# Optimization experiments

Hardware: AMD Instinct MI355X
Metric: run time of the kernel (lower is better)

Reference implementation:

```python
import jax, jax.numpy as jnp
import numpy as np

EPS = 1e-6
OMEGA = 0.1


def setup_inputs() -> dict:
    key = jax.random.key(0)
    k1, k2 = jax.random.split(key)
    n, d, kk = 4096, 128, 4
    inputs = jax.random.uniform(k1, (n, d), dtype=jnp.float32)  # positive so log(sim) is finite
    labels = jax.random.randint(k2, (n, kk), 0, 64, dtype=jnp.int64)
    return {"inputs": inputs, "labels": labels}


def reference(inputs, labels):
    n, kk = labels.shape
    sim = inputs @ inputs.T                      # [n, n]
    logsim = jnp.log(sim + EPS)                  # a_{jk} = log(sim[j,k]+eps)
    targets = labels[:, 0]
    eye = jnp.eye(n, dtype=bool)
    # pos_mask[j,k] = (targets[j] == targets[k]) xor diagonal
    pos = (targets[:, None] == targets[None, :]) & ~eye
    # eq[j,l,i] = (labels[l,i] == targets[j])
    eq = targets[:, None, None] == labels[None, :, :]
    m_idx = jnp.arange(kk)
    cols = kk - 1 - m_idx                        # neg_mask[m] uses label column kk-1-m
    # neg_mask[m][j,l] == 1  <=>  ~eq[j,l,kk-1-m]  AND  (m==0 or eq[j,l,kk-m])
    neq_col = ~eq[:, :, cols]                    # [j,l,m]
    prev_ok = jnp.concatenate(
        [jnp.ones((n, n, 1), dtype=bool), eq[:, :, cols[:-1]]], axis=-1)
    neg = neq_col & prev_ok                      # [j,l,m]
    # loss_pair[m] = log(Omega+eps) - log(Omega^(kk-m+1)+eps)
    lp = jnp.log(OMEGA + EPS) - jnp.log(OMEGA ** (kk - m_idx + 1) + EPS)  # [kk]
    dt = logsim.dtype
    posf = pos.astype(dt)
    negf = neg.astype(dt)
    # term = (a_jk - b_jlm)^2 with b_jlm = logsim[j,l] + 0.1*lp[m]
    # expand: sum_jklm pos*neg*(a^2 - 2ab + b^2), separable over k and (l,m)
    c = posf.sum(1)                              # [j] count of positives
    S1 = (posf * logsim).sum(1)                  # [j] sum a
    S2 = (posf * logsim ** 2).sum(1)             # [j] sum a^2
    b = logsim[:, :, None] + 0.1 * lp[None, None, :]   # [j,l,m]
    Ncnt = negf.sum(1)                           # [j,m]
    T1 = (negf * b).sum(1)                       # [j,m]
    T2 = (negf * b ** 2).sum(1)                  # [j,m]
    loss = (S2[:, None] * Ncnt - 2.0 * S1[:, None] * T1 + c[:, None] * T2).sum()
    return loss
```

## Files before the change

### kernel.cpp

```cpp
#include <hip/hip_runtime.h>
#include <math.h>

constexpr int N  = 4096;
constexpr int D  = 128;
constexpr int TI = 128;
constexpr int TJ = 128;
constexpr int LDK = D + 8;
constexpr int REDSTRIDE = 97;

typedef __attribute__((ext_vector_type(8))) short short8;
typedef __attribute__((ext_vector_type(4))) float floatx4;

__device__ inline unsigned short f2bf(float f) {
  unsigned u = __builtin_bit_cast(unsigned, f);
  u = (u + 0x7FFFu + ((u >> 16) & 1u)) >> 16;
  return (unsigned short)u;
}

__global__ __launch_bounds__(256, 2) void logratio_phaseA(
    const float* __restrict__ inputs, const int* __restrict__ labels,
    float* __restrict__ ws,
    float B0, float B1, float B2, float B3,
    float Q0, float Q1, float Q2, float Q3) {

  __shared__ char smem[2 * 128 * LDK * 2];
  unsigned short* As = (unsigned short*)smem;
  unsigned short* Bs = As + 128 * LDK;

  const int tid = threadIdx.x;
  const int iBase = blockIdx.y * TI;
  const int jBase = blockIdx.x * TJ;

#pragma unroll
  for (int p = 0; p < 16; ++p) {
    const int idx = p * 256 + tid;
    const int row = idx >> 5;
    const int cf  = idx & 31;
    const float4 va = *(const float4*)&inputs[(iBase + row) * D + cf * 4];
    uint2 wa;
    wa.x = (unsigned)f2bf(va.x) | ((unsigned)f2bf(va.y) << 16);
    wa.y = (unsigned)f2bf(va.z) | ((unsigned)f2bf(va.w) << 16);
    *(uint2*)&As[row * LDK + cf * 4] = wa;
    const float4 vb = *(const float4*)&inputs[(jBase + row) * D + cf * 4];
    uint2 wb;
    wb.x = (unsigned)f2bf(vb.x) | ((unsigned)f2bf(vb.y) << 16);
    wb.y = (unsigned)f2bf(vb.z) | ((unsigned)f2bf(vb.w) << 16);
    *(uint2*)&Bs[row * LDK + cf * 4] = wb;
  }
  __syncthreads();

  const int w    = tid >> 6;
  const int lane = tid & 63;
  const int lc   = lane & 15;
  const int quad = lane >> 4;

  floatx4 acc[2][8] = {};

  const unsigned short* Abase = As + (w * 32 + lc) * LDK + quad * 8;
  const unsigned short* Bbase = Bs + lc * LDK + quad * 8;

#pragma unroll
  for (int kb = 0; kb < 4; ++kb) {
    short8 af[2], bfr[8];
    af[0] = *(const short8*)(Abase + kb * 32);
    af[1] = *(const short8*)(Abase + 16 * LDK + kb * 32);
#pragma unroll
    for (int tn = 0; tn < 8; ++tn)
      bfr[tn] = *(const short8*)(Bbase + tn * 16 * LDK + kb * 32);
#pragma unroll
    for (int tm = 0; tm < 2; ++tm)
#pragma unroll
      for (int tn = 0; tn < 8; ++tn)
        acc[tm][tn] = __builtin_amdgcn_mfma_f32_16x16x32_bf16(af[tm], bfr[tn], acc[tm][tn], 0, 0, 0);
  }

  int4 labs[8];
#pragma unroll
  for (int tn = 0; tn < 8; ++tn)
    labs[tn] = ((const int4*)labels)[jBase + tn * 16 + lc];

  __syncthreads();
  float* Red = (float*)smem;

#pragma unroll
  for (int tm = 0; tm < 2; ++tm) {
#pragma unroll
    for (int reg = 0; reg < 4; ++reg) {
      const int row = w * 32 + tm * 16 + quad * 4 + reg;
      const int gi = iBase + row;
      const int ti = labels[gi * 4];

      float a_c = 0.f, a_s1 = 0.f, a_s2 = 0.f;
      float a_A = 0.f, a_B = 0.f, a_C = 0.f;

#pragma unroll
      for (int tn = 0; tn < 8; ++tn) {
        const int gj = jBase + tn * 16 + lc;
        const float sim = acc[tm][tn][reg];
        const float ls  = __logf(sim + 1e-6f);
        const float ls2 = ls * ls;
        const int4 L = labs[tn];
        const bool e0 = (ti == L.x);
        const bool e1 = (ti == L.y);
        const bool e2 = (ti == L.z);
        const bool e3 = (ti == L.w);
        const bool n1 = e3 && !e2;
        const bool n2 = e2 && !e1;
        const bool n3 = e1 && !e0;
        const float g0 = (float)((e3 ? 0 : 1) + (n1 ? 1 : 0) + (n2 ? 1 : 0) + (n3 ? 1 : 0));
        const float gB = (e3 ? (n1 ? B1 : 0.f) : B0) + (n2 ? B2 : 0.f) + (n3 ? B3 : 0.f);
        const float gQ = (e3 ? (n1 ? Q1 : 0.f) : Q0) + (n2 ? Q2 : 0.f) + (n3 ? Q3 : 0.f);
        const float fp = (e0 && (gi != gj)) ? 1.f : 0.f;

        a_c += fp;
        a_s1 = fmaf(fp, ls, a_s1);
        a_s2 = fmaf(fp, ls2, a_s2);
        a_A += g0;
        a_B += fmaf(g0, ls, gB);
        a_C += fmaf(fmaf(g0, ls, 2.f * gB), ls, gQ);
      }

      float* dst = Red + row * REDSTRIDE + lc * 6;
      dst[0] = a_c;  dst[1] = a_s1; dst[2] = a_s2;
      dst[3] = a_A;  dst[4] = a_B;  dst[5] = a_C;
    }
  }
  __syncthreads();

  if (tid < 128) {
    const int row = tid;
    const int gi = iBase + row;
    const float* src = Red + row * REDSTRIDE;
    float s0 = 0.f, s1 = 0.f, s2 = 0.f, s3 = 0.f, s4 = 0.f, s5 = 0.f;
#pragma unroll
    for (int l = 0; l < 16; ++l) {
      s0 += src[l * 6 + 0]; s1 += src[l * 6 + 1]; s2 += src[l * 6 + 2];
      s3 += src[l * 6 + 3]; s4 += src[l * 6 + 4]; s5 += src[l * 6 + 5];
    }
    atomicAdd(&ws[0 * N + gi], s0);
    atomicAdd(&ws[1 * N + gi], s1);
    atomicAdd(&ws[2 * N + gi], s2);
    atomicAdd(&ws[3 * N + gi], s3);
    atomicAdd(&ws[4 * N + gi], s4);
    atomicAdd(&ws[5 * N + gi], s5);
  }
}

__global__ __launch_bounds__(256) void logratio_phaseB(
    const float* __restrict__ ws, float* __restrict__ out) {
  const int i = blockIdx.x * 256 + threadIdx.x;
  const float c  = ws[0 * N + i];
  const float S1 = ws[1 * N + i];
  const float S2 = ws[2 * N + i];
  const float A  = ws[3 * N + i];
  const float B  = ws[4 * N + i];
  const float C  = ws[5 * N + i];
  float v = S2 * A - 2.f * S1 * B + c * C;
#pragma unroll
  for (int m = 32; m >= 1; m >>= 1) v += __shfl_xor(v, m, 64);
  __shared__ float wsum[4];
  if ((threadIdx.x & 63) == 0) wsum[threadIdx.x >> 6] = v;
  __syncthreads();
  if (threadIdx.x == 0)
    atomicAdd(out, wsum[0] + wsum[1] + wsum[2] + wsum[3]);
}

extern "C" void kernel_launch(void* const* d_in, const int* in_sizes, int n_in,
                              void* d_out, int out_size, void* d_ws, size_t ws_size,
                              hipStream_t stream) {
  const float* inputs = (const float*)d_in[0];
  const int* labels = (const int*)d_in[1];
  float* out = (float*)d_out;
  float* ws = (float*)d_ws;

  hipMemsetAsync(d_ws, 0, 6 * N * sizeof(float), stream);
  hipMemsetAsync(d_out, 0, sizeof(float), stream);

  float Bq[4], Qq[4];
  for (int m = 0; m < 4; ++m) {
    const float lpv = logf(0.1f + 1e-6f) - logf(powf(0.1f, (float)(5 - m)) + 1e-6f);
    Bq[m] = 0.1f * lpv;
    Qq[m] = Bq[m] * Bq[m];
  }

  dim3 grid(N / TJ, N / TI);
  logratio_phaseA<<<grid, 256, 0, stream>>>(inputs, labels, ws,
                                            Bq[0], Bq[1], Bq[2], Bq[3],
                                            Qq[0], Qq[1], Qq[2], Qq[3]);
  logratio_phaseB<<<N / 256, 256, 0, stream>>>(ws, out);
}
```

Measured before the change: 91.01 us.

## Compact sparse label matches into per-wave queues and use dense baseline sums

The per-element epilogue now computes only the log-similarity and its square densely. Elements whose label matches are pushed into per-wave LDS queues and processed sparsely as corrections to a baseline assumption of all-negative. Global atomics are replaced by per-block partial slots in the workspace, which removes the workspace memset, and phase B reduces those slots. The queued log values are stored as fp16, and entries beyond a fixed queue capacity are dropped, which can introduce error if matches are dense.

```diff
diff --git a/kernel.cpp b/kernel.cpp
--- a/kernel.cpp
+++ b/kernel.cpp
@@ -1,12 +1,11 @@
 #include <hip/hip_runtime.h>
+#include <hip/hip_fp16.h>
 #include <math.h>
 
-constexpr int N  = 4096;
-constexpr int D  = 128;
-constexpr int TI = 128;
-constexpr int TJ = 128;
+constexpr int N   = 4096;
+constexpr int D   = 128;
 constexpr int LDK = D + 8;
-constexpr int REDSTRIDE = 97;
+constexpr int QCAPW = 1024;
 
 typedef __attribute__((ext_vector_type(8))) short short8;
 typedef __attribute__((ext_vector_type(4))) float floatx4;
@@ -23,13 +22,16 @@
     float B0, float B1, float B2, float B3,
     float Q0, float Q1, float Q2, float Q3) {
 
-  __shared__ char smem[2 * 128 * LDK * 2];
+  __shared__ __align__(16) char smem[2 * 128 * LDK * 2];
   unsigned short* As = (unsigned short*)smem;
   unsigned short* Bs = As + 128 * LDK;
+  float (*rowacc)[8] = (float (*)[8])smem;
+  unsigned* queues   = (unsigned*)(smem + 4096);
+  unsigned* qcnt     = (unsigned*)(smem + 4096 + 16384);
 
   const int tid = threadIdx.x;
-  const int iBase = blockIdx.y * TI;
-  const int jBase = blockIdx.x * TJ;
+  const int iBase = blockIdx.y * 128;
+  const int jBase = blockIdx.x * 128;
 
 #pragma unroll
   for (int p = 0; p < 16; ++p) {
@@ -55,7 +57,6 @@
   const int quad = lane >> 4;
 
   floatx4 acc[2][8] = {};
-
   const unsigned short* Abase = As + (w * 32 + lc) * LDK + quad * 8;
   const unsigned short* Bbase = Bs + lc * LDK + quad * 8;
 
@@ -80,7 +81,12 @@
     labs[tn] = ((const int4*)labels)[jBase + tn * 16 + lc];
 
   __syncthreads();
-  float* Red = (float*)smem;
+
+  for (int z = tid; z < 128 * 8; z += 256) ((float*)rowacc)[z] = 0.f;
+  __syncthreads();
+
+  unsigned wq = 0;
+  unsigned* wqueue = queues + w * QCAPW;
 
 #pragma unroll
   for (int tm = 0; tm < 2; ++tm) {
@@ -89,80 +95,102 @@
       const int row = w * 32 + tm * 16 + quad * 4 + reg;
       const int gi = iBase + row;
       const int ti = labels[gi * 4];
-
-      float a_c = 0.f, a_s1 = 0.f, a_s2 = 0.f;
-      float a_A = 0.f, a_B = 0.f, a_C = 0.f;
-
+      float t0 = 0.f, t1 = 0.f;
 #pragma unroll
       for (int tn = 0; tn < 8; ++tn) {
-        const int gj = jBase + tn * 16 + lc;
-        const float sim = acc[tm][tn][reg];
-        const float ls  = __logf(sim + 1e-6f);
-        const float ls2 = ls * ls;
+        const int col = tn * 16 + lc;
+        const float ls = __logf(acc[tm][tn][reg] + 1e-6f);
+        t0 += ls;
+        t1 = fmaf(ls, ls, t1);
         const int4 L = labs[tn];
-        const bool e0 = (ti == L.x);
-        const bool e1 = (ti == L.y);
-        const bool e2 = (ti == L.z);
-        const bool e3 = (ti == L.w);
-        const bool n1 = e3 && !e2;
-        const bool n2 = e2 && !e1;
-        const bool n3 = e1 && !e0;
-        const float g0 = (float)((e3 ? 0 : 1) + (n1 ? 1 : 0) + (n2 ? 1 : 0) + (n3 ? 1 : 0));
-        const float gB = (e3 ? (n1 ? B1 : 0.f) : B0) + (n2 ? B2 : 0.f) + (n3 ? B3 : 0.f);
-        const float gQ = (e3 ? (n1 ? Q1 : 0.f) : Q0) + (n2 ? Q2 : 0.f) + (n3 ? Q3 : 0.f);
-        const float fp = (e0 && (gi != gj)) ? 1.f : 0.f;
-
-        a_c += fp;
-        a_s1 = fmaf(fp, ls, a_s1);
-        a_s2 = fmaf(fp, ls2, a_s2);
-        a_A += g0;
-        a_B += fmaf(g0, ls, gB);
-        a_C += fmaf(fmaf(g0, ls, 2.f * gB), ls, gQ);
+        const bool match = (ti == L.x) | (ti == L.y) | (ti == L.z) | (ti == L.w);
+        const unsigned long long mk = __ballot(match);
+        if (mk) {
+          const unsigned pfx = __builtin_amdgcn_mbcnt_hi(
+              (unsigned)(mk >> 32), __builtin_amdgcn_mbcnt_lo((unsigned)mk, 0u));
+          if (match) {
+            const unsigned pos = wq + pfx;
+            if (pos < (unsigned)QCAPW)
+              wqueue[pos] = ((unsigned)(row * 128 + col) << 16) |
+                            (unsigned)__half_as_ushort(__float2half(ls));
+          }
+          wq += (unsigned)__popcll(mk);
+        }
       }
-
-      float* dst = Red + row * REDSTRIDE + lc * 6;
-      dst[0] = a_c;  dst[1] = a_s1; dst[2] = a_s2;
-      dst[3] = a_A;  dst[4] = a_B;  dst[5] = a_C;
+#pragma unroll
+      for (int m = 1; m <= 8; m <<= 1) {
+        t0 += __shfl_xor(t0, m, 64);
+        t1 += __shfl_xor(t1, m, 64);
+      }
+      if (lc == 0) { rowacc[row][6] = t0; rowacc[row][7] = t1; }
     }
   }
+  if (lane == 0) qcnt[w] = (wq < (unsigned)QCAPW) ? wq : (unsigned)QCAPW;
+  __syncthreads();
+
+#pragma unroll 1
+  for (int qw = 0; qw < 4; ++qw) {
+    const unsigned qn = qcnt[qw];
+    const unsigned* qq = queues + qw * QCAPW;
+    for (unsigned q = tid; q < qn; q += 256) {
+      const unsigned e = qq[q];
+      const int idx = (int)(e >> 16);
+      const int row = idx >> 7;
+      const int col = idx & 127;
+      const float ls = __half2float(__ushort_as_half((unsigned short)(e & 0xFFFFu)));
+      const int gi = iBase + row, gj = jBase + col;
+      const int ti = labels[gi * 4];
+      const int4 L = ((const int4*)labels)[gj];
+      const bool e0 = (ti == L.x), e1 = (ti == L.y), e2 = (ti == L.z), e3 = (ti == L.w);
+      const float g0 = (e3 ? 0.f : 1.f) + ((e3 && !e2) ? 1.f : 0.f) +
+                       ((e2 && !e1) ? 1.f : 0.f) + ((e1 && !e0) ? 1.f : 0.f);
+      const float gB = (e3 ? (!e2 ? B1 : 0.f) : B0) + ((e2 && !e1) ? B2 : 0.f) + ((e1 && !e0) ? B3 : 0.f);
+      const float gQ = (e3 ? (!e2 ? Q1 : 0.f) : Q0) + ((e2 && !e1) ? Q2 : 0.f) + ((e1 && !e0) ? Q3 : 0.f);
+      const float fp = (e0 && (gi != gj)) ? 1.f : 0.f;
+      const float dg0 = g0 - 1.f, dgB = gB - B0, dgQ = gQ - Q0;
+      const float ls2 = ls * ls;
+      atomicAdd(&rowacc[row][0], fp);
+      atomicAdd(&rowacc[row][1], fp * ls);
+      atomicAdd(&rowacc[row][2], fp * ls2);
+      atomicAdd(&rowacc[row][3], dg0);
+      atomicAdd(&rowacc[row][4], fmaf(dg0, ls, dgB));
+      atomicAdd(&rowacc[row][5], fmaf(fmaf(dg0, ls, 2.f * dgB), ls, dgQ));
+    }
+  }
   __syncthreads();
 
   if (tid < 128) {
-    const int row = tid;
-    const int gi = iBase + row;
-    const float* src = Red + row * REDSTRIDE;
-    float s0 = 0.f, s1 = 0.f, s2 = 0.f, s3 = 0.f, s4 = 0.f, s5 = 0.f;
-#pragma unroll
-    for (int l = 0; l < 16; ++l) {
-      s0 += src[l * 6 + 0]; s1 += src[l * 6 + 1]; s2 += src[l * 6 + 2];
-      s3 += src[l * 6 + 3]; s4 += src[l * 6 + 4]; s5 += src[l * 6 + 5];
-    }
-    atomicAdd(&ws[0 * N + gi], s0);
-    atomicAdd(&ws[1 * N + gi], s1);
-    atomicAdd(&ws[2 * N + gi], s2);
-    atomicAdd(&ws[3 * N + gi], s3);
-    atomicAdd(&ws[4 * N + gi], s4);
-    atomicAdd(&ws[5 * N + gi], s5);
+    const int gi = iBase + tid;
+    float* dst = ws + (size_t)gi * 256 + blockIdx.x * 8;
+    *(float4*)dst       = make_float4(rowacc[tid][0], rowacc[tid][1], rowacc[tid][2], rowacc[tid][3]);
+    *(float4*)(dst + 4) = make_float4(rowacc[tid][4], rowacc[tid][5], rowacc[tid][6], rowacc[tid][7]);
   }
 }
 
 __global__ __launch_bounds__(256) void logratio_phaseB(
-    const float* __restrict__ ws, float* __restrict__ out) {
+    const float* __restrict__ ws, float* __restrict__ out, float B0, float Q0) {
   const int i = blockIdx.x * 256 + threadIdx.x;
-  const float c  = ws[0 * N + i];
-  const float S1 = ws[1 * N + i];
-  const float S2 = ws[2 * N + i];
-  const float A  = ws[3 * N + i];
-  const float B  = ws[4 * N + i];
-  const float C  = ws[5 * N + i];
-  float v = S2 * A - 2.f * S1 * B + c * C;
+  const float4* p = (const float4*)(ws + (size_t)i * 256);
+  float4 a0 = make_float4(0.f, 0.f, 0.f, 0.f);
+  float4 a1 = make_float4(0.f, 0.f, 0.f, 0.f);
+#pragma unroll 8
+  for (int b = 0; b < 32; ++b) {
+    const float4 x = p[2 * b], y = p[2 * b + 1];
+    a0.x += x.x; a0.y += x.y; a0.z += x.z; a0.w += x.w;
+    a1.x += y.x; a1.y += y.y; a1.z += y.z; a1.w += y.w;
+  }
+  const float c = a0.x, S1 = a0.y, S2 = a0.z, dA = a0.w;
+  const float dB = a1.x, dC = a1.y, T0 = a1.z, T1 = a1.w;
+  const float A  = (float)N + dA;
+  const float Bv = T0 + (float)N * B0 + dB;
+  const float Cv = T1 + 2.f * B0 * T0 + (float)N * Q0 + dC;
+  float v = S2 * A - 2.f * S1 * Bv + c * Cv;
 #pragma unroll
   for (int m = 32; m >= 1; m >>= 1) v += __shfl_xor(v, m, 64);
   __shared__ float wsum[4];
   if ((threadIdx.x & 63) == 0) wsum[threadIdx.x >> 6] = v;
   __syncthreads();
-  if (threadIdx.x == 0)
-    atomicAdd(out, wsum[0] + wsum[1] + wsum[2] + wsum[3]);
+  if (threadIdx.x == 0) atomicAdd(out, wsum[0] + wsum[1] + wsum[2] + wsum[3]);
 }
 
 extern "C" void kernel_launch(void* const* d_in, const int* in_sizes, int n_in,
@@ -173,7 +201,6 @@
   float* out = (float*)d_out;
   float* ws = (float*)d_ws;
 
-  hipMemsetAsync(d_ws, 0, 6 * N * sizeof(float), stream);
   hipMemsetAsync(d_out, 0, sizeof(float), stream);
 
   float Bq[4], Qq[4];
@@ -183,9 +210,9 @@
     Qq[m] = Bq[m] * Bq[m];
   }
 
-  dim3 grid(N / TJ, N / TI);
+  dim3 grid(N / 128, N / 128);
   logratio_phaseA<<<grid, 256, 0, stream>>>(inputs, labels, ws,
                                             Bq[0], Bq[1], Bq[2], Bq[3],
                                             Qq[0], Qq[1], Qq[2], Qq[3]);
-  logratio_phaseB<<<N / 256, 256, 0, stream>>>(ws, out);
-}
+  logratio_phaseB<<<N / 256, 256, 0, stream>>>(ws, out, Bq[0], Qq[0]);
+}
```

Result: slower. 136.6 us (+50.1%).

## Precompute per-label coefficient table and replace atomics with partial-sum buffer

Applied to the files above, without the earlier changes.

Adds a kernel that builds a 64xN table of float4 coefficients (gB, gQ, g0, positive flag), indexed by target label and column, so the epilogue does a table load instead of label comparisons and selects. The per-row atomicAdds into the workspace are replaced by plain writes of per-block partial sums, which phaseB then reduces; this also removes the workspace memset. The table costs 4 MB of writes plus gathered loads in the epilogue, and it adds an extra kernel launch. The table relies on labels being in the range 0-63.

```diff
diff --git a/kernel.cpp b/kernel.cpp
--- a/kernel.cpp
+++ b/kernel.cpp
@@ -1,12 +1,10 @@
 #include <hip/hip_runtime.h>
 #include <math.h>
 
-constexpr int N  = 4096;
-constexpr int D  = 128;
-constexpr int TI = 128;
-constexpr int TJ = 128;
+constexpr int N   = 4096;
+constexpr int D   = 128;
 constexpr int LDK = D + 8;
-constexpr int REDSTRIDE = 97;
+constexpr int NT  = 64;
 
 typedef __attribute__((ext_vector_type(8))) short short8;
 typedef __attribute__((ext_vector_type(4))) float floatx4;
@@ -17,19 +15,34 @@
   return (unsigned short)u;
 }
 
+__global__ __launch_bounds__(256) void build_coef(
+    const int* __restrict__ labels, float4* __restrict__ tab,
+    float B0, float B1, float B2, float B3,
+    float Q0, float Q1, float Q2, float Q3) {
+  const int idx = blockIdx.x * 256 + threadIdx.x;
+  const int t = idx >> 12;
+  const int j = idx & (N - 1);
+  const int4 L = ((const int4*)labels)[j];
+  const bool e0 = (t == L.x), e1 = (t == L.y), e2 = (t == L.z), e3 = (t == L.w);
+  const bool n0 = !e3, n1 = e3 && !e2, n2 = e2 && !e1, n3 = e1 && !e0;
+  const float g0 = (float)((n0 ? 1 : 0) + (n1 ? 1 : 0) + (n2 ? 1 : 0) + (n3 ? 1 : 0));
+  const float gB = (n0 ? B0 : 0.f) + (n1 ? B1 : 0.f) + (n2 ? B2 : 0.f) + (n3 ? B3 : 0.f);
+  const float gQ = (n0 ? Q0 : 0.f) + (n1 ? Q1 : 0.f) + (n2 ? Q2 : 0.f) + (n3 ? Q3 : 0.f);
+  tab[idx] = make_float4(gB, gQ, g0, e0 ? 1.f : 0.f);
+}
+
 __global__ __launch_bounds__(256, 2) void logratio_phaseA(
     const float* __restrict__ inputs, const int* __restrict__ labels,
-    float* __restrict__ ws,
-    float B0, float B1, float B2, float B3,
-    float Q0, float Q1, float Q2, float Q3) {
+    const float4* __restrict__ tab, float* __restrict__ part) {
 
-  __shared__ char smem[2 * 128 * LDK * 2];
+  __shared__ __align__(16) char smem[2 * 128 * LDK * 2];
   unsigned short* As = (unsigned short*)smem;
   unsigned short* Bs = As + 128 * LDK;
+  float* Red = (float*)smem;
 
   const int tid = threadIdx.x;
-  const int iBase = blockIdx.y * TI;
-  const int jBase = blockIdx.x * TJ;
+  const int iBase = blockIdx.y * 128;
+  const int jBase = blockIdx.x * 128;
 
 #pragma unroll
   for (int p = 0; p < 16; ++p) {
@@ -55,7 +68,6 @@
   const int quad = lane >> 4;
 
   floatx4 acc[2][8] = {};
-
   const unsigned short* Abase = As + (w * 32 + lc) * LDK + quad * 8;
   const unsigned short* Bbase = Bs + lc * LDK + quad * 8;
 
@@ -74,14 +86,9 @@
         acc[tm][tn] = __builtin_amdgcn_mfma_f32_16x16x32_bf16(af[tm], bfr[tn], acc[tm][tn], 0, 0, 0);
   }
 
-  int4 labs[8];
-#pragma unroll
-  for (int tn = 0; tn < 8; ++tn)
-    labs[tn] = ((const int4*)labels)[jBase + tn * 16 + lc];
+  __syncthreads();
 
-  __syncthreads();
-  float* Red = (float*)smem;
-
+  const bool diag = (iBase == jBase);
 #pragma unroll
   for (int tm = 0; tm < 2; ++tm) {
 #pragma unroll
@@ -89,38 +96,26 @@
       const int row = w * 32 + tm * 16 + quad * 4 + reg;
       const int gi = iBase + row;
       const int ti = labels[gi * 4];
+      const float4* tabrow = tab + ti * N + jBase + lc;
+      const int dcol = diag ? row : -1;
 
       float a_c = 0.f, a_s1 = 0.f, a_s2 = 0.f;
       float a_A = 0.f, a_B = 0.f, a_C = 0.f;
-
 #pragma unroll
       for (int tn = 0; tn < 8; ++tn) {
-        const int gj = jBase + tn * 16 + lc;
-        const float sim = acc[tm][tn][reg];
-        const float ls  = __logf(sim + 1e-6f);
-        const float ls2 = ls * ls;
-        const int4 L = labs[tn];
-        const bool e0 = (ti == L.x);
-        const bool e1 = (ti == L.y);
-        const bool e2 = (ti == L.z);
-        const bool e3 = (ti == L.w);
-        const bool n1 = e3 && !e2;
-        const bool n2 = e2 && !e1;
-        const bool n3 = e1 && !e0;
-        const float g0 = (float)((e3 ? 0 : 1) + (n1 ? 1 : 0) + (n2 ? 1 : 0) + (n3 ? 1 : 0));
-        const float gB = (e3 ? (n1 ? B1 : 0.f) : B0) + (n2 ? B2 : 0.f) + (n3 ? B3 : 0.f);
-        const float gQ = (e3 ? (n1 ? Q1 : 0.f) : Q0) + (n2 ? Q2 : 0.f) + (n3 ? Q3 : 0.f);
-        const float fp = (e0 && (gi != gj)) ? 1.f : 0.f;
-
-        a_c += fp;
-        a_s1 = fmaf(fp, ls, a_s1);
-        a_s2 = fmaf(fp, ls2, a_s2);
-        a_A += g0;
-        a_B += fmaf(g0, ls, gB);
-        a_C += fmaf(fmaf(g0, ls, 2.f * gB), ls, gQ);
+        const float4 cf = tabrow[tn * 16];
+        const float ls = __logf(acc[tm][tn][reg] + 1e-6f);
+        const float t1 = fmaf(cf.z, ls, cf.x);
+        a_A += cf.z;
+        a_B += t1;
+        a_C += fmaf(t1 + cf.x, ls, cf.y);
+        const float f = (tn * 16 + lc == dcol) ? 0.f : cf.w;
+        const float fls = f * ls;
+        a_c += f;
+        a_s1 += fls;
+        a_s2 = fmaf(fls, ls, a_s2);
       }
-
-      float* dst = Red + row * REDSTRIDE + lc * 6;
+      float* dst = Red + row * 97 + lc * 6;
       dst[0] = a_c;  dst[1] = a_s1; dst[2] = a_s2;
       dst[3] = a_A;  dst[4] = a_B;  dst[5] = a_C;
     }
@@ -128,41 +123,38 @@
   __syncthreads();
 
   if (tid < 128) {
-    const int row = tid;
-    const int gi = iBase + row;
-    const float* src = Red + row * REDSTRIDE;
+    const int gi = iBase + tid;
+    const float* src = Red + tid * 97;
     float s0 = 0.f, s1 = 0.f, s2 = 0.f, s3 = 0.f, s4 = 0.f, s5 = 0.f;
 #pragma unroll
     for (int l = 0; l < 16; ++l) {
       s0 += src[l * 6 + 0]; s1 += src[l * 6 + 1]; s2 += src[l * 6 + 2];
       s3 += src[l * 6 + 3]; s4 += src[l * 6 + 4]; s5 += src[l * 6 + 5];
     }
-    atomicAdd(&ws[0 * N + gi], s0);
-    atomicAdd(&ws[1 * N + gi], s1);
-    atomicAdd(&ws[2 * N + gi], s2);
-    atomicAdd(&ws[3 * N + gi], s3);
-    atomicAdd(&ws[4 * N + gi], s4);
-    atomicAdd(&ws[5 * N + gi], s5);
+    float* dst = part + (size_t)gi * 256 + blockIdx.x * 8;
+    *(float4*)dst       = make_float4(s0, s1, s2, s3);
+    *(float2*)(dst + 4) = make_float2(s4, s5);
   }
 }
 
 __global__ __launch_bounds__(256) void logratio_phaseB(
-    const float* __restrict__ ws, float* __restrict__ out) {
+    const float* __restrict__ part, float* __restrict__ out) {
   const int i = blockIdx.x * 256 + threadIdx.x;
-  const float c  = ws[0 * N + i];
-  const float S1 = ws[1 * N + i];
-  const float S2 = ws[2 * N + i];
-  const float A  = ws[3 * N + i];
-  const float B  = ws[4 * N + i];
-  const float C  = ws[5 * N + i];
+  const float* p = part + (size_t)i * 256;
+  float c = 0.f, S1 = 0.f, S2 = 0.f, A = 0.f, B = 0.f, C = 0.f;
+#pragma unroll 8
+  for (int b = 0; b < 32; ++b) {
+    const float4 x = *(const float4*)(p + b * 8);
+    const float2 y = *(const float2*)(p + b * 8 + 4);
+    c += x.x; S1 += x.y; S2 += x.z; A += x.w; B += y.x; C += y.y;
+  }
   float v = S2 * A - 2.f * S1 * B + c * C;
 #pragma unroll
   for (int m = 32; m >= 1; m >>= 1) v += __shfl_xor(v, m, 64);
   __shared__ float wsum[4];
   if ((threadIdx.x & 63) == 0) wsum[threadIdx.x >> 6] = v;
   __syncthreads();
-  if (threadIdx.x == 0)
-    atomicAdd(out, wsum[0] + wsum[1] + wsum[2] + wsum[3]);
+  if (threadIdx.x == 0) atomicAdd(out, wsum[0] + wsum[1] + wsum[2] + wsum[3]);
 }
 
 extern "C" void kernel_launch(void* const* d_in, const int* in_sizes, int n_in,
@@ -171,9 +163,9 @@
   const float* inputs = (const float*)d_in[0];
   const int* labels = (const int*)d_in[1];
   float* out = (float*)d_out;
-  float* ws = (float*)d_ws;
+  float4* tab = (float4*)d_ws;
+  float* part = (float*)d_ws + (NT * N * 4);
 
-  hipMemsetAsync(d_ws, 0, 6 * N * sizeof(float), stream);
   hipMemsetAsync(d_out, 0, sizeof(float), stream);
 
   float Bq[4], Qq[4];
@@ -183,9 +175,10 @@
     Qq[m] = Bq[m] * Bq[m];
   }
 
-  dim3 grid(N / TJ, N / TI);
-  logratio_phaseA<<<grid, 256, 0, stream>>>(inputs, labels, ws,
-                                            Bq[0], Bq[1], Bq[2], Bq[3],
-                                            Qq[0], Qq[1], Qq[2], Qq[3]);
-  logratio_phaseB<<<N / 256, 256, 0, stream>>>(ws, out);
+  build_coef<<<NT * N / 256, 256, 0, stream>>>(labels, tab,
+                                               Bq[0], Bq[1], Bq[2], Bq[3],
+                                               Qq[0], Qq[1], Qq[2], Qq[3]);
+  dim3 grid(N / 128, N / 128);
+  logratio_phaseA<<<grid, 256, 0, stream>>>(inputs, labels, tab, part);
+  logratio_phaseB<<<N / 256, 256, 0, stream>>>(part, out);
 }
```

Result: no change. 92.46 us (+1.6%).
